# Optimization experiments

Measured on AMD Instinct MI355X. Metric: run time of the kernel, lower is better.

Reference implementation:

```python
import jax, jax.numpy as jnp
import numpy as np

N_PER_VIEW = 8192
N_VIEWS = 3
N = N_PER_VIEW * N_VIEWS  # 24576 homogeneous nodes
E = 393216
R = 6          # num_relations
B = 8          # num_bases
PROJ = 128     # proj_dim
HEADS = 4
OUT = 32
HO = HEADS * OUT  # 128
LABELS = 4
NEG_SLOPE = 0.2


def setup_inputs() -> dict:
    key = jax.random.key(0)
    ks = jax.random.split(key, 32)
    inp = {}
    inp["x0"] = jax.random.normal(ks[0], (N_PER_VIEW, 2000), jnp.float32)
    inp["x1"] = jax.random.normal(ks[1], (N_PER_VIEW, 1500), jnp.float32)
    inp["x2"] = jax.random.normal(ks[2], (N_PER_VIEW, 500), jnp.float32)
    inp["edge_index"] = jax.random.randint(ks[3], (2, E), 0, N, jnp.int32)
    inp["edge_type"] = jax.random.randint(ks[4], (E,), 0, R, jnp.int32)
    # per-view projection params (pyg.nn.Linear: y = x @ W.T + b)
    inp["Wp0"] = jax.random.normal(ks[5], (PROJ, 2000), jnp.float32) * 0.02
    inp["bp0"] = jnp.zeros((PROJ,), jnp.float32)
    inp["Wp1"] = jax.random.normal(ks[6], (PROJ, 1500), jnp.float32) * 0.02
    inp["bp1"] = jnp.zeros((PROJ,), jnp.float32)
    inp["Wp2"] = jax.random.normal(ks[7], (PROJ, 500), jnp.float32) * 0.02
    inp["bp2"] = jnp.zeros((PROJ,), jnp.float32)
    # RGATConv layer 0 (in = PROJ = 128)
    inp["basis0"] = jax.random.normal(ks[8], (B, PROJ, HO), jnp.float32) * 0.05
    inp["comp0"] = jax.random.normal(ks[9], (R, B), jnp.float32) * 0.3
    inp["q0"] = jax.random.normal(ks[10], (HO, HEADS), jnp.float32) * 0.1
    inp["k0"] = jax.random.normal(ks[11], (HO, HEADS), jnp.float32) * 0.1
    # RGATConv layer 1 (in = HO = 128)
    inp["basis1"] = jax.random.normal(ks[12], (B, HO, HO), jnp.float32) * 0.05
    inp["comp1"] = jax.random.normal(ks[13], (R, B), jnp.float32) * 0.3
    inp["q1"] = jax.random.normal(ks[14], (HO, HEADS), jnp.float32) * 0.1
    inp["k1"] = jax.random.normal(ks[15], (HO, HEADS), jnp.float32) * 0.1
    # LinearIntegration: concat views -> Linear(n_views*HO, n_classes)
    inp["Wc"] = jax.random.normal(ks[16], (LABELS, N_VIEWS * HO), jnp.float32) * 0.05
    inp["bc"] = jnp.zeros((LABELS,), jnp.float32)
    return inp


def _rgat_layer(x, src, dst, edge_type, basis, comp, q, k):
    """PyG RGATConv: basis-decomposed weights, additive self-attention,
    within-relation softmax, mod='f-scaled', heads concatenated."""
    w = jnp.einsum('rb,bio->rio', comp, basis)          # [R, in, H*O]
    xw = jnp.einsum('ni,rio->rno', x, w)                # [R, N, H*O]
    out_j = xw[edge_type, src]                          # [E, H*O] (source msg)
    out_i = xw[edge_type, dst]                          # [E, H*O] (target)
    alpha = jax.nn.leaky_relu(out_i @ q + out_j @ k, NEG_SLOPE)  # [E, H]
    # within-relation softmax over edges sharing (relation, dst)
    seg = edge_type.astype(jnp.int32) * N + dst
    nseg = R * N
    amax = jax.ops.segment_max(alpha, seg, num_segments=nseg)
    ex = jnp.exp(alpha - amax[seg])
    den = jax.ops.segment_sum(ex, seg, num_segments=nseg)
    a = ex / (den[seg] + 1e-16)
    # mod='f-scaled': scale by destination in-degree (over all relations)
    deg = jax.ops.segment_sum(jnp.ones((E,), x.dtype), dst, num_segments=N)
    a = a * deg[dst][:, None]
    msg = (a[:, :, None] * out_j.reshape(E, HEADS, OUT)).reshape(E, HO)
    return jax.ops.segment_sum(msg, dst, num_segments=N)  # [N, H*O]


def _forward(x0, x1, x2, Wp0, bp0, Wp1, bp1, Wp2, bp2,
             basis0, comp0, q0, k0, basis1, comp1, q1, k1, Wc, bc,
             src, dst, edge_type):
    h0 = jax.nn.relu(x0 @ Wp0.T + bp0)
    h1 = jax.nn.relu(x1 @ Wp1.T + bp1)
    h2 = jax.nn.relu(x2 @ Wp2.T + bp2)
    x = jnp.concatenate([h0, h1, h2], axis=0)           # [N, PROJ]
    x = _rgat_layer(x, src, dst, edge_type, basis0, comp0, q0, k0)
    x = _rgat_layer(x, src, dst, edge_type, basis1, comp1, q1, k1)
    views = x.reshape(N_VIEWS, N_PER_VIEW, HO)          # nodes grouped by view
    feat = jnp.transpose(views, (1, 0, 2)).reshape(N_PER_VIEW, N_VIEWS * HO)
    return feat @ Wc.T + bc                              # [N_per_view, LABELS]


def reference(x0, x1, x2, edge_index, edge_type, Wp0, bp0, Wp1, bp1, Wp2, bp2,
              basis0, comp0, q0, k0, basis1, comp1, q1, k1, Wc, bc):
    src, dst = edge_index[0], edge_index[1]
    return _forward(x0, x1, x2, Wp0, bp0, Wp1, bp1, Wp2, bp2,
                    basis0, comp0, q0, k0, basis1, comp1, q1, k1, Wc, bc,
                    src, dst, edge_type)
```

## Files before the change

kernel.cpp:

```cpp
#include <hip/hip_runtime.h>
#include <hip/hip_bf16.h>
#include <math.h>

#define N_NODES 24576
#define NPV 8192
#define E_EDGES 393216
#define R_REL 6
#define B_BASES 8
#define HEADS 4
#define NEG_SLOPE 0.2f
#define NX (N_NODES * 128)
#define NK (N_NODES * R_REL)
#define SCAN_BLOCKS (NK / 256)

typedef unsigned short ushort_t;
using short8 = __attribute__((ext_vector_type(8))) short;
using f32x4 = __attribute__((ext_vector_type(4))) float;

__device__ __forceinline__ float lrelu(float x) { return x >= 0.f ? x : NEG_SLOPE * x; }
__device__ __forceinline__ float b2f(ushort_t u) {
  unsigned int v = ((unsigned int)u) << 16;
  float f;
  __builtin_memcpy(&f, &v, 4);
  return f;
}
__device__ __forceinline__ ushort_t f2b(float f) {
  __hip_bfloat16 h = __float2bfloat16(f);
  ushort_t u;
  __builtin_memcpy(&u, &h, 2);
  return u;
}

__global__ __launch_bounds__(256) void gemm_proj(
    const float* __restrict__ x0, const float* __restrict__ x1,
    const float* __restrict__ x2, const float* __restrict__ w0,
    const float* __restrict__ w1, const float* __restrict__ w2,
    const float* __restrict__ b0, const float* __restrict__ b1,
    const float* __restrict__ b2, ushort_t* __restrict__ xb) {
  __shared__ __align__(16) ushort_t As[64 * 64];
  __shared__ __align__(16) ushort_t Ws[128 * 64];
  const int v = blockIdx.y;
  const float* A;
  const float* W;
  const float* bias;
  int K;
  if (v == 0) { A = x0; W = w0; bias = b0; K = 2000; }
  else if (v == 1) { A = x1; W = w1; bias = b1; K = 1500; }
  else { A = x2; W = w2; bias = b2; K = 500; }
  const int tid = threadIdx.x;
  const int wave = tid >> 6, lane = tid & 63;
  const int m0 = blockIdx.x * 64;

  f32x4 acc[8];
#pragma unroll
  for (int n = 0; n < 8; ++n) acc[n] = (f32x4){0.f, 0.f, 0.f, 0.f};

  const int nsteps = (K + 63) >> 6;
  for (int step = 0; step < nsteps; ++step) {
    const int k0 = step << 6;
    __syncthreads();
#pragma unroll
    for (int q = 0; q < 2; ++q) {
      int s = q * 256 + tid;
      int row = s >> 3, ch = s & 7;
      int gk = k0 + ((ch ^ (row & 7)) << 3);
      const float* gp = A + (long)(m0 + row) * K + gk;
      short8 o;
      if (gk + 8 <= K) {
        float4 a = *reinterpret_cast<const float4*>(gp);
        float4 b = *reinterpret_cast<const float4*>(gp + 4);
        o[0] = (short)f2b(a.x); o[1] = (short)f2b(a.y);
        o[2] = (short)f2b(a.z); o[3] = (short)f2b(a.w);
        o[4] = (short)f2b(b.x); o[5] = (short)f2b(b.y);
        o[6] = (short)f2b(b.z); o[7] = (short)f2b(b.w);
      } else {
#pragma unroll
        for (int j = 0; j < 8; ++j)
          o[j] = (gk + j < K) ? (short)f2b(gp[j]) : (short)0;
      }
      *reinterpret_cast<short8*>(As + s * 8) = o;
    }
#pragma unroll
    for (int q = 0; q < 4; ++q) {
      int s = q * 256 + tid;
      int row = s >> 3, ch = s & 7;
      int gk = k0 + ((ch ^ (row & 7)) << 3);
      const float* gp = W + (long)row * K + gk;
      short8 o;
      if (gk + 8 <= K) {
        float4 a = *reinterpret_cast<const float4*>(gp);
        float4 b = *reinterpret_cast<const float4*>(gp + 4);
        o[0] = (short)f2b(a.x); o[1] = (short)f2b(a.y);
        o[2] = (short)f2b(a.z); o[3] = (short)f2b(a.w);
        o[4] = (short)f2b(b.x); o[5] = (short)f2b(b.y);
        o[6] = (short)f2b(b.z); o[7] = (short)f2b(b.w);
      } else {
#pragma unroll
        for (int j = 0; j < 8; ++j)
          o[j] = (gk + j < K) ? (short)f2b(gp[j]) : (short)0;
      }
      *reinterpret_cast<short8*>(Ws + s * 8) = o;
    }
    __syncthreads();
#pragma unroll
    for (int kk = 0; kk < 2; ++kk) {
      const int arow = wave * 16 + (lane & 15);
      const int ach = (kk * 4 + (lane >> 4)) ^ (arow & 7);
      short8 afrag = *reinterpret_cast<const short8*>(As + arow * 64 + ach * 8);
#pragma unroll
      for (int n = 0; n < 8; ++n) {
        const int brow = n * 16 + (lane & 15);
        const int bch = (kk * 4 + (lane >> 4)) ^ (brow & 7);
        short8 bfrag = *reinterpret_cast<const short8*>(Ws + brow * 64 + bch * 8);
        acc[n] = __builtin_amdgcn_mfma_f32_16x16x32_bf16(afrag, bfrag, acc[n], 0, 0, 0);
      }
    }
  }
  const int rbase = m0 + wave * 16 + (lane >> 4) * 4;
  const int cb = lane & 15;
  ushort_t* out = xb + (long)v * NPV * 128;
#pragma unroll
  for (int n = 0; n < 8; ++n) {
    int col = n * 16 + cb;
    float bz = bias[col];
#pragma unroll
    for (int r = 0; r < 4; ++r) {
      float val = acc[n][r] + bz;
      val = val > 0.f ? val : 0.f;
      out[(long)(rbase + r) * 128 + col] = f2b(val);
    }
  }
}

template <bool SPLIT, bool TABLES>
__global__ __launch_bounds__(256) void mfma_gemm_nt(
    const ushort_t* __restrict__ A, const ushort_t* __restrict__ W,
    float* __restrict__ Cacc, ushort_t* __restrict__ Cb,
    int Kp, int kChunk, long strideW, long strideCz,
    const float* __restrict__ qt, const float* __restrict__ kt,
    float* __restrict__ ai, float* __restrict__ aj) {
  __shared__ __align__(16) ushort_t As[64 * 64];
  __shared__ __align__(16) ushort_t Ws[128 * 64];
  const int tid = threadIdx.x;
  const int wave = tid >> 6, lane = tid & 63;
  const int m0 = blockIdx.x * 64;
  const int kbase = blockIdx.y * kChunk;
  const ushort_t* Wz = W + (long)blockIdx.z * strideW;

  f32x4 acc[8];
#pragma unroll
  for (int n = 0; n < 8; ++n) acc[n] = (f32x4){0.f, 0.f, 0.f, 0.f};

  for (int k0 = kbase; k0 < kbase + kChunk; k0 += 64) {
    __syncthreads();
#pragma unroll
    for (int q = 0; q < 2; ++q) {
      int s = q * 256 + tid;
      int row = s >> 3, ch = s & 7;
      int sch = ch ^ (row & 7);
      const ushort_t* g = A + (long)(m0 + row) * Kp + k0 + sch * 8;
      __builtin_amdgcn_global_load_lds(
          (const __attribute__((address_space(1))) unsigned int*)g,
          (__attribute__((address_space(3))) unsigned int*)(As + s * 8), 16, 0, 0);
    }
#pragma unroll
    for (int q = 0; q < 4; ++q) {
      int s = q * 256 + tid;
      int row = s >> 3, ch = s & 7;
      int sch = ch ^ (row & 7);
      const ushort_t* g = Wz + (long)row * Kp + k0 + sch * 8;
      __builtin_amdgcn_global_load_lds(
          (const __attribute__((address_space(1))) unsigned int*)g,
          (__attribute__((address_space(3))) unsigned int*)(Ws + s * 8), 16, 0, 0);
    }
    __syncthreads();
#pragma unroll
    for (int kk = 0; kk < 2; ++kk) {
      const int arow = wave * 16 + (lane & 15);
      const int ach = (kk * 4 + (lane >> 4)) ^ (arow & 7);
      short8 afrag = *reinterpret_cast<const short8*>(As + arow * 64 + ach * 8);
#pragma unroll
      for (int n = 0; n < 8; ++n) {
        const int brow = n * 16 + (lane & 15);
        const int bch = (kk * 4 + (lane >> 4)) ^ (brow & 7);
        short8 bfrag = *reinterpret_cast<const short8*>(Ws + brow * 64 + bch * 8);
        acc[n] = __builtin_amdgcn_mfma_f32_16x16x32_bf16(afrag, bfrag, acc[n], 0, 0, 0);
      }
    }
  }
  const int rbase = m0 + wave * 16 + (lane >> 4) * 4;
  const int cb = lane & 15;
  if (SPLIT) {
#pragma unroll
    for (int n = 0; n < 8; ++n) {
      int col = n * 16 + cb;
#pragma unroll
      for (int r = 0; r < 4; ++r)
        atomicAdd(&Cacc[(long)(rbase + r) * 128 + col], acc[n][r]);
    }
  } else {
    ushort_t* Cz = Cb + (long)blockIdx.z * strideCz;
#pragma unroll
    for (int n = 0; n < 8; ++n) {
      int col = n * 16 + cb;
#pragma unroll
      for (int r = 0; r < 4; ++r)
        Cz[(long)(rbase + r) * 128 + col] = f2b(acc[n][r]);
    }
  }
  if (TABLES) {
    float aq[4][4], ak[4][4];
#pragma unroll
    for (int r = 0; r < 4; ++r)
#pragma unroll
      for (int h = 0; h < 4; ++h) { aq[r][h] = 0.f; ak[r][h] = 0.f; }
#pragma unroll
    for (int n = 0; n < 8; ++n) {
      int col = n * 16 + cb;
      float4 qv = *reinterpret_cast<const float4*>(qt + (long)col * 4);
      float4 kv = *reinterpret_cast<const float4*>(kt + (long)col * 4);
#pragma unroll
      for (int r = 0; r < 4; ++r) {
        float x = acc[n][r];
        aq[r][0] += x * qv.x; aq[r][1] += x * qv.y;
        aq[r][2] += x * qv.z; aq[r][3] += x * qv.w;
        ak[r][0] += x * kv.x; ak[r][1] += x * kv.y;
        ak[r][2] += x * kv.z; ak[r][3] += x * kv.w;
      }
    }
#pragma unroll
    for (int mk = 1; mk < 16; mk <<= 1) {
#pragma unroll
      for (int r = 0; r < 4; ++r)
#pragma unroll
        for (int h = 0; h < 4; ++h) {
          aq[r][h] += __shfl_xor(aq[r][h], mk);
          ak[r][h] += __shfl_xor(ak[r][h], mk);
        }
    }
    int rr = cb >> 2, hh = cb & 3;
    long row = (long)blockIdx.z * N_NODES + rbase + rr;
    ai[row * 4 + hh] = aq[rr][hh];
    aj[row * 4 + hh] = ak[rr][hh];
  }
}

__global__ void fill_f32(float* __restrict__ p, long n, float v) {
  long i = blockIdx.x * (long)blockDim.x + threadIdx.x;
  long stride = (long)gridDim.x * blockDim.x;
  for (; i < n; i += stride) p[i] = v;
}

__global__ void compute_wT_b(const float* __restrict__ comp,
                             const float* __restrict__ basis,
                             ushort_t* __restrict__ wTb) {
  int idx = blockIdx.x * blockDim.x + threadIdx.x;
  if (idx >= R_REL * 128 * 128) return;
  int r = idx >> 14;
  int rem = idx & 16383;
  int o = rem >> 7;
  int i = rem & 127;
  float s = 0.f;
#pragma unroll
  for (int b = 0; b < B_BASES; ++b)
    s += comp[r * B_BASES + b] * basis[((b << 7) + i) * 128 + o];
  wTb[((long)(r << 7) + o) * 128 + i] = f2b(s);
}

__global__ void count_key(const int* __restrict__ dst, const int* __restrict__ et,
                          int* __restrict__ cnt, int E) {
  int e = blockIdx.x * blockDim.x + threadIdx.x;
  if (e < E) atomicAdd(&cnt[dst[e] * R_REL + et[e]], 1);
}

__global__ __launch_bounds__(256) void scan_block(const int* __restrict__ cnt,
                                                  int* __restrict__ start,
                                                  int* __restrict__ blockSums) {
  __shared__ int sm[256];
  const int t = threadIdx.x;
  const int i = blockIdx.x * 256 + t;
  int v = cnt[i];
  sm[t] = v;
  __syncthreads();
  for (int off = 1; off < 256; off <<= 1) {
    int u = (t >= off) ? sm[t - off] : 0;
    __syncthreads();
    sm[t] += u;
    __syncthreads();
  }
  start[i] = sm[t] - v;
  if (t == 255) blockSums[blockIdx.x] = sm[255];
}

__global__ __launch_bounds__(SCAN_BLOCKS) void scan_sums(int* __restrict__ blockSums) {
  __shared__ int sm[SCAN_BLOCKS];
  const int t = threadIdx.x;
  int v = blockSums[t];
  sm[t] = v;
  __syncthreads();
  for (int off = 1; off < SCAN_BLOCKS; off <<= 1) {
    int u = (t >= off) ? sm[t - off] : 0;
    __syncthreads();
    sm[t] += u;
    __syncthreads();
  }
  blockSums[t] = sm[t] - v;
}

__global__ __launch_bounds__(256) void add_offsets(int* __restrict__ start,
                                                   const int* __restrict__ blockSums) {
  int i = blockIdx.x * 256 + threadIdx.x;
  start[i] += blockSums[blockIdx.x];
  if (i == 0) start[NK] = E_EDGES;
}

__global__ void scatter_edges(const int* __restrict__ src, const int* __restrict__ dst,
                              const int* __restrict__ et, const int* __restrict__ start,
                              int* __restrict__ cursor, int* __restrict__ recs, int E) {
  int e = blockIdx.x * blockDim.x + threadIdx.x;
  if (e >= E) return;
  int key = dst[e] * R_REL + et[e];
  int pos = start[key] + atomicAdd(&cursor[key], 1);
  recs[pos] = src[e] | (et[e] << 16);
}

__global__ __launch_bounds__(256) void seg_softmax(
    const int* __restrict__ rstart, const int* __restrict__ recs,
    const float* __restrict__ ai, const float* __restrict__ aj,
    float* __restrict__ coef) {
  int seg = blockIdx.x * blockDim.x + threadIdx.x;
  if (seg >= NK) return;
  int p0 = rstart[seg], p1 = rstart[seg + 1];
  if (p0 == p1) return;
  int d = seg / R_REL, r = seg - d * R_REL;
  float4 av = *reinterpret_cast<const float4*>(ai + ((long)r * N_NODES + d) * 4);
  float degf = (float)(rstart[(d + 1) * R_REL] - rstart[d * R_REL]);
  float m[4] = {-INFINITY, -INFINITY, -INFINITY, -INFINITY};
  float sum[4] = {0.f, 0.f, 0.f, 0.f};
  for (int p = p0; p < p1; ++p) {
    int s = recs[p] & 0xFFFF;
    float4 bv = *reinterpret_cast<const float4*>(aj + ((long)r * N_NODES + s) * 4);
    float al[4] = {lrelu(av.x + bv.x), lrelu(av.y + bv.y),
                   lrelu(av.z + bv.z), lrelu(av.w + bv.w)};
#pragma unroll
    for (int h = 0; h < 4; ++h) {
      float nm = fmaxf(m[h], al[h]);
      sum[h] = sum[h] * __expf(m[h] - nm) + __expf(al[h] - nm);
      m[h] = nm;
    }
  }
  float rs[4];
#pragma unroll
  for (int h = 0; h < 4; ++h) rs[h] = degf / (sum[h] + 1e-16f);
  for (int p = p0; p < p1; ++p) {
    int s = recs[p] & 0xFFFF;
    float4 bv = *reinterpret_cast<const float4*>(aj + ((long)r * N_NODES + s) * 4);
    float al[4] = {lrelu(av.x + bv.x), lrelu(av.y + bv.y),
                   lrelu(av.z + bv.z), lrelu(av.w + bv.w)};
#pragma unroll
    for (int h = 0; h < 4; ++h)
      coef[(long)h * E_EDGES + p] = __expf(al[h] - m[h]) * rs[h];
  }
}

__global__ __launch_bounds__(256) void fused_agg(
    const int* __restrict__ rstart, const int* __restrict__ recs,
    const float* __restrict__ coef, const ushort_t* __restrict__ xwb,
    ushort_t* __restrict__ xb_out, float* __restrict__ fout) {
  const int wave = threadIdx.x >> 6, lane = threadIdx.x & 63;
  const int d = blockIdx.x * 4 + wave;
  const int s0 = rstart[d * R_REL], s1 = rstart[(d + 1) * R_REL];
  const float* cfp = coef + (long)(lane >> 4) * E_EDGES;
  float acc0 = 0.f, acc1 = 0.f;
#pragma unroll 4
  for (int pos = s0; pos < s1; ++pos) {
    int rec = recs[pos];
    float cf = cfp[pos];
    int s = rec & 0xFFFF, r = rec >> 16;
    unsigned int pk = *reinterpret_cast<const unsigned int*>(
        xwb + (((long)r * N_NODES + s) << 7) + 2 * lane);
    acc0 += cf * b2f((ushort_t)(pk & 0xFFFF));
    acc1 += cf * b2f((ushort_t)(pk >> 16));
  }
  if (xb_out) {
    unsigned int po = ((unsigned int)f2b(acc1) << 16) | (unsigned int)f2b(acc0);
    *reinterpret_cast<unsigned int*>(xb_out + ((long)d << 7) + 2 * lane) = po;
  }
  if (fout) {
    *reinterpret_cast<float2*>(fout + ((long)d << 7) + 2 * lane) =
        make_float2(acc0, acc1);
  }
}

__global__ void final_linear(const float* __restrict__ x, const float* __restrict__ Wc,
                             const float* __restrict__ bc, float* __restrict__ out) {
  __shared__ float wcs[4 * 384];
  for (int t = threadIdx.x; t < 4 * 384; t += blockDim.x) wcs[t] = Wc[t];
  __syncthreads();
  int i = blockIdx.x * blockDim.x + threadIdx.x;
  if (i >= NPV) return;
  float acc[4] = {0.f, 0.f, 0.f, 0.f};
  for (int v = 0; v < 3; ++v) {
    const float* xr = x + ((long)v * NPV + i) * 128;
    for (int c = 0; c < 128; c += 4) {
      float4 xv = *reinterpret_cast<const float4*>(xr + c);
#pragma unroll
      for (int l = 0; l < 4; ++l) {
        const float* w = wcs + l * 384 + v * 128 + c;
        acc[l] += xv.x * w[0] + xv.y * w[1] + xv.z * w[2] + xv.w * w[3];
      }
    }
  }
#pragma unroll
  for (int l = 0; l < 4; ++l) out[(long)i * 4 + l] = acc[l] + bc[l];
}

static void run_layer(const ushort_t* xb_in, ushort_t* xb_out, float* fout,
                      const float* basis, const float* comp, const float* q,
                      const float* k, ushort_t* xwb, ushort_t* wTb, float* ai,
                      float* aj, float* coef, const int* rstart, const int* recs,
                      hipStream_t stream) {
  compute_wT_b<<<(R_REL * 128 * 128 + 255) / 256, 256, 0, stream>>>(comp, basis, wTb);
  mfma_gemm_nt<false, true><<<dim3(N_NODES / 64, 1, R_REL), 256, 0, stream>>>(
      xb_in, wTb, nullptr, xwb, 128, 128, 128 * 128, (long)N_NODES * 128,
      q, k, ai, aj);
  seg_softmax<<<(NK + 255) / 256, 256, 0, stream>>>(rstart, recs, ai, aj, coef);
  fused_agg<<<N_NODES / 4, 256, 0, stream>>>(rstart, recs, coef, xwb, xb_out, fout);
}

extern "C" void kernel_launch(void* const* d_in, const int* in_sizes, int n_in,
                              void* d_out, int out_size, void* d_ws, size_t ws_size,
                              hipStream_t stream) {
  const float* x0 = (const float*)d_in[0];
  const float* x1 = (const float*)d_in[1];
  const float* x2 = (const float*)d_in[2];
  const int* edge_index = (const int*)d_in[3];
  const int* edge_type = (const int*)d_in[4];
  const float* Wp0 = (const float*)d_in[5];
  const float* bp0 = (const float*)d_in[6];
  const float* Wp1 = (const float*)d_in[7];
  const float* bp1 = (const float*)d_in[8];
  const float* Wp2 = (const float*)d_in[9];
  const float* bp2 = (const float*)d_in[10];
  const float* basis0 = (const float*)d_in[11];
  const float* comp0 = (const float*)d_in[12];
  const float* q0 = (const float*)d_in[13];
  const float* k0 = (const float*)d_in[14];
  const float* basis1 = (const float*)d_in[15];
  const float* comp1 = (const float*)d_in[16];
  const float* q1 = (const float*)d_in[17];
  const float* k1 = (const float*)d_in[18];
  const float* Wc = (const float*)d_in[19];
  const float* bc = (const float*)d_in[20];

  const int* src = edge_index;
  const int* dst = edge_index + E_EDGES;

  char* w = (char*)d_ws;
  auto alloc = [&](long bytes) {
    char* p = w;
    w += (bytes + 255) & ~255L;
    return p;
  };
  ushort_t* xbA  = (ushort_t*)alloc((long)NX * 2);
  ushort_t* xbB  = (ushort_t*)alloc((long)NX * 2);
  ushort_t* xwb  = (ushort_t*)alloc((long)R_REL * NX * 2);
  ushort_t* wTb  = (ushort_t*)alloc((long)R_REL * 128 * 128 * 2);
  float* Cacc    = (float*)alloc((long)NX * 4);
  float* ai      = (float*)alloc((long)R_REL * N_NODES * 4 * 4);
  float* aj      = (float*)alloc((long)R_REL * N_NODES * 4 * 4);
  float* coef    = (float*)alloc((long)HEADS * E_EDGES * 4);
  int* cnt       = (int*)alloc((long)NK * 4);
  int* cursor    = (int*)alloc((long)NK * 4);
  int* rstart    = (int*)alloc((long)(NK + 1) * 4);
  int* recs      = (int*)alloc((long)E_EDGES * 4);
  int* blockSums = (int*)alloc((long)SCAN_BLOCKS * 4);

  gemm_proj<<<dim3(NPV / 64, 3), 256, 0, stream>>>(
      x0, x1, x2, Wp0, Wp1, Wp2, bp0, bp1, bp2, xbA);

  fill_f32<<<96, 256, 0, stream>>>((float*)cnt, 2L * NK, 0.f);
  count_key<<<E_EDGES / 256, 256, 0, stream>>>(dst, edge_type, cnt, E_EDGES);
  scan_block<<<SCAN_BLOCKS, 256, 0, stream>>>(cnt, rstart, blockSums);
  scan_sums<<<1, SCAN_BLOCKS, 0, stream>>>(blockSums);
  add_offsets<<<SCAN_BLOCKS, 256, 0, stream>>>(rstart, blockSums);
  scatter_edges<<<E_EDGES / 256, 256, 0, stream>>>(src, dst, edge_type, rstart,
                                                   cursor, recs, E_EDGES);

  run_layer(xbA, xbB, nullptr, basis0, comp0, q0, k0, xwb, wTb, ai, aj, coef,
            rstart, recs, stream);
  run_layer(xbB, nullptr, Cacc, basis1, comp1, q1, k1, xwb, wTb, ai, aj, coef,
            rstart, recs, stream);

  final_linear<<<(NPV + 255) / 256, 256, 0, stream>>>(Cacc, Wc, bc, (float*)d_out);
}
```

Measured before the change: 315.8 us.

## Split-K the view projection GEMM across 9 blocks with a reduce kernel

The per-view projection GEMM previously ran 128x3 blocks, with view 0 looping over the full K=2000 while view 2 covered only 500, which gave poor load balance and low occupancy. It now splits K into 9 chunks of at most 512, writing fp32 partial sums into a reused workspace. A new reduce kernel then adds bias, applies ReLU and converts to bf16. This buys more parallelism and balanced blocks at the cost of extra fp32 partial traffic and one more launch.

```diff
diff --git a/kernel.cpp b/kernel.cpp
--- a/kernel.cpp
+++ b/kernel.cpp
@@ -31,22 +31,20 @@
   return u;
 }
 
-__global__ __launch_bounds__(256) void gemm_proj(
+__global__ __launch_bounds__(256) void gemm_proj_split(
     const float* __restrict__ x0, const float* __restrict__ x1,
     const float* __restrict__ x2, const float* __restrict__ w0,
     const float* __restrict__ w1, const float* __restrict__ w2,
-    const float* __restrict__ b0, const float* __restrict__ b1,
-    const float* __restrict__ b2, ushort_t* __restrict__ xb) {
+    float* __restrict__ Ppart) {
   __shared__ __align__(16) ushort_t As[64 * 64];
   __shared__ __align__(16) ushort_t Ws[128 * 64];
-  const int v = blockIdx.y;
+  const int z = blockIdx.y;
   const float* A;
   const float* W;
-  const float* bias;
-  int K;
-  if (v == 0) { A = x0; W = w0; bias = b0; K = 2000; }
-  else if (v == 1) { A = x1; W = w1; bias = b1; K = 1500; }
-  else { A = x2; W = w2; bias = b2; K = 500; }
+  int K, kstart, ksteps;
+  if (z < 4)      { A = x0; W = w0; K = 2000; kstart = z * 512;       ksteps = 8; }
+  else if (z < 7) { A = x1; W = w1; K = 1500; kstart = (z - 4) * 512; ksteps = 8; }
+  else            { A = x2; W = w2; K = 500;  kstart = (z - 7) * 256; ksteps = 4; }
   const int tid = threadIdx.x;
   const int wave = tid >> 6, lane = tid & 63;
   const int m0 = blockIdx.x * 64;
@@ -55,9 +53,8 @@
 #pragma unroll
   for (int n = 0; n < 8; ++n) acc[n] = (f32x4){0.f, 0.f, 0.f, 0.f};
 
-  const int nsteps = (K + 63) >> 6;
-  for (int step = 0; step < nsteps; ++step) {
-    const int k0 = step << 6;
+  for (int step = 0; step < ksteps; ++step) {
+    const int k0 = kstart + (step << 6);
     __syncthreads();
 #pragma unroll
     for (int q = 0; q < 2; ++q) {
@@ -118,18 +115,46 @@
   }
   const int rbase = m0 + wave * 16 + (lane >> 4) * 4;
   const int cb = lane & 15;
-  ushort_t* out = xb + (long)v * NPV * 128;
+  float* out = Ppart + (long)z * NPV * 128;
 #pragma unroll
   for (int n = 0; n < 8; ++n) {
     int col = n * 16 + cb;
-    float bz = bias[col];
-#pragma unroll
-    for (int r = 0; r < 4; ++r) {
-      float val = acc[n][r] + bz;
-      val = val > 0.f ? val : 0.f;
-      out[(long)(rbase + r) * 128 + col] = f2b(val);
-    }
-  }
+#pragma unroll
+    for (int r = 0; r < 4; ++r)
+      out[(long)(rbase + r) * 128 + col] = acc[n][r];
+  }
+}
+
+__global__ __launch_bounds__(256) void proj_reduce(
+    const float* __restrict__ Ppart, const float* __restrict__ b0,
+    const float* __restrict__ b1, const float* __restrict__ b2,
+    ushort_t* __restrict__ xb) {
+  int t = blockIdx.x * blockDim.x + threadIdx.x;
+  if (t >= N_NODES * 16) return;
+  int n = t >> 4, c0 = (t & 15) * 8;
+  int v = n >> 13, m = n & (NPV - 1);
+  int zb, zc;
+  const float* bias;
+  if (v == 0) { zb = 0; zc = 4; bias = b0; }
+  else if (v == 1) { zb = 4; zc = 3; bias = b1; }
+  else { zb = 7; zc = 2; bias = b2; }
+  float s[8];
+#pragma unroll
+  for (int j = 0; j < 8; ++j) s[j] = bias[c0 + j];
+  for (int zz = 0; zz < zc; ++zz) {
+    const float* p = Ppart + ((long)(zb + zz) * NPV + m) * 128 + c0;
+    float4 a = *reinterpret_cast<const float4*>(p);
+    float4 b = *reinterpret_cast<const float4*>(p + 4);
+    s[0] += a.x; s[1] += a.y; s[2] += a.z; s[3] += a.w;
+    s[4] += b.x; s[5] += b.y; s[6] += b.z; s[7] += b.w;
+  }
+  short8 o;
+#pragma unroll
+  for (int j = 0; j < 8; ++j) {
+    float vv = s[j] > 0.f ? s[j] : 0.f;
+    o[j] = (short)f2b(vv);
+  }
+  *reinterpret_cast<short8*>(xb + (long)n * 128 + c0) = o;
 }
 
 template <bool SPLIT, bool TABLES>
@@ -464,7 +489,7 @@
   };
   ushort_t* xbA  = (ushort_t*)alloc((long)NX * 2);
   ushort_t* xbB  = (ushort_t*)alloc((long)NX * 2);
-  ushort_t* xwb  = (ushort_t*)alloc((long)R_REL * NX * 2);
+  ushort_t* xwb  = (ushort_t*)alloc(9L * NPV * 128 * 4);
   ushort_t* wTb  = (ushort_t*)alloc((long)R_REL * 128 * 128 * 2);
   float* Cacc    = (float*)alloc((long)NX * 4);
   float* ai      = (float*)alloc((long)R_REL * N_NODES * 4 * 4);
@@ -475,9 +500,12 @@
   int* rstart    = (int*)alloc((long)(NK + 1) * 4);
   int* recs      = (int*)alloc((long)E_EDGES * 4);
   int* blockSums = (int*)alloc((long)SCAN_BLOCKS * 4);
-
-  gemm_proj<<<dim3(NPV / 64, 3), 256, 0, stream>>>(
-      x0, x1, x2, Wp0, Wp1, Wp2, bp0, bp1, bp2, xbA);
+  float* Ppart   = (float*)xwb;
+
+  gemm_proj_split<<<dim3(NPV / 64, 9), 256, 0, stream>>>(
+      x0, x1, x2, Wp0, Wp1, Wp2, Ppart);
+  proj_reduce<<<(N_NODES * 16 + 255) / 256, 256, 0, stream>>>(
+      Ppart, bp0, bp1, bp2, xbA);
 
   fill_f32<<<96, 256, 0, stream>>>((float*)cnt, 2L * NK, 0.f);
   count_key<<<E_EDGES / 256, 256, 0, stream>>>(dst, edge_type, cnt, E_EDGES);
```

Result: faster. 278.5 us (-11.8%).
